# Performance work log

Hardware: AMD Instinct MI355X
Metric: run time of the kernel (lower is better)

## Reference

```python
import jax, jax.numpy as jnp
import numpy as np
jax.config.update('jax_enable_x64', True)

B, T, D = 4, 4096, 1024
H, NX = 16, 16          # num_heads, num_x_bits
NV = D // H             # num_v_bits = 64


def setup_inputs() -> dict:
    key = jax.random.key(0)
    ks = jax.random.split(key, 4)
    s = 1.0 / np.sqrt(D)
    x = jax.random.normal(ks[0], (B, T, D), dtype=jnp.float32)
    Wq = jax.random.uniform(ks[1], (H * NX, D), jnp.float32, -s, s)
    Wk = jax.random.uniform(ks[2], (H * NX, D), jnp.float32, -s, s)
    Wv = jax.random.uniform(ks[3], (H * NV, D), jnp.float32, -s, s)
    emb0 = jnp.full((D,), -1e-5, dtype=jnp.float32)
    emb1 = jnp.full((D,), +1e-5, dtype=jnp.float32)
    return {"x": x, "Wq": Wq, "Wk": Wk, "Wv": Wv, "emb0": emb0, "emb1": emb1}


def _pack_bits(z, nb):
    # z: (B,T,H*nb) -> int64 codes (B,H,T); bit i set iff z_bit_i > 0
    bits = (z > 0).reshape(B, T, H, nb).transpose(0, 2, 1, 3).astype(jnp.int64)
    w = jnp.left_shift(jnp.int64(1), jnp.arange(nb, dtype=jnp.int64))
    return jnp.sum(bits * w, axis=-1)


def _rosa_lookup(qc, kc, vc):
    # Hash-based causal exact-match lookup (inferred semantics of
    # torch_rosa.rosa_qkv_fwd): y[t] = v[j] for the latest j < t with
    # k-code[j] == q-code[t], else 0.  qc,kc,vc: (BH, T) int64.
    BH = qc.shape[0]
    rows = jnp.arange(BH)
    table = jnp.zeros((BH, 1 << NX), dtype=jnp.int64)

    def step(tab, inp):
        qt, kt, vt = inp  # (BH,)
        y = tab[rows, qt]
        tab = tab.at[rows, kt].set(vt)
        return tab, y

    _, ys = jax.lax.scan(step, table, (qc.T, kc.T, vc.T))
    return ys.T  # (BH, T)


def reference(x, Wq, Wk, Wv, emb0, emb1):
    q = x @ Wq.T  # (B,T,H*NX)
    k = x @ Wk.T
    v = x @ Wv.T  # (B,T,H*NV)
    qc = _pack_bits(q, NX).reshape(-1, T)
    kc = _pack_bits(k, NX).reshape(-1, T)
    vc = _pack_bits(v, NV).reshape(-1, T)
    y = _rosa_lookup(qc, kc, vc).reshape(B, H, T)
    rv = jnp.arange(NV, dtype=jnp.int64)
    m = ((y[..., None] >> rv) & 1).astype(bool)      # (B,H,T,NV)
    m = m.transpose(0, 2, 1, 3).reshape(B, T, D)      # (B,T,D)
    return jnp.where(m, emb1, emb0)
```

## Files before the change

### kernel.cpp

```cpp
#include <hip/hip_runtime.h>
#include <stdint.h>

#define B_   4
#define T_   4096
#define D_   1024
#define H_   16
#define M_   16384
#define NTOT 1536
#define BM   64
#define BN   64
#define BK   32
#define KC   384

typedef unsigned short u16;
typedef unsigned long long u64;

__device__ __forceinline__ float bf16r(float f) {
    unsigned int u = __float_as_uint(f);
    u += 0x7FFFu + ((u >> 16) & 1u);
    return __uint_as_float(u & 0xFFFF0000u);
}

__global__ __launch_bounds__(256) void gemm_pack_kernel(
    const float* __restrict__ x, const float* __restrict__ Wq,
    const float* __restrict__ Wk, const float* __restrict__ Wv,
    u16* __restrict__ qc, u16* __restrict__ kc, u64* __restrict__ vc)
{
    __shared__ float As[BM][BK + 1];
    __shared__ float Bs[BK][BN + 4];
    __shared__ unsigned char sub[BM][16];

    const int tid = threadIdx.x;
    const int tx = tid & 15, ty = tid >> 4;
    const int m0 = blockIdx.x * BM;
    const int n0 = blockIdx.y * BN;

    const float* Wsrc; int f0;
    if (n0 < 256)      { Wsrc = Wq; f0 = n0; }
    else if (n0 < 512) { Wsrc = Wk; f0 = n0 - 256; }
    else               { Wsrc = Wv; f0 = n0 - 512; }

    float run[4][4], tot[4][4];
    #pragma unroll
    for (int i = 0; i < 4; ++i)
        #pragma unroll
        for (int j = 0; j < 4; ++j) { run[i][j] = 0.f; tot[i][j] = 0.f; }

    const int r8 = tid >> 2;
    const int c8 = (tid & 3) * 8;

    for (int k0 = 0; k0 < D_; k0 += BK) {
        const float* xp = x + (size_t)(m0 + r8) * D_ + k0 + c8;
        float4 a0 = *(const float4*)xp, a1 = *(const float4*)(xp + 4);
        const float* wp = Wsrc + (size_t)(f0 + r8) * D_ + k0 + c8;
        float4 w0 = *(const float4*)wp, w1 = *(const float4*)(wp + 4);
        As[r8][c8 + 0] = a0.x; As[r8][c8 + 1] = a0.y;
        As[r8][c8 + 2] = a0.z; As[r8][c8 + 3] = a0.w;
        As[r8][c8 + 4] = a1.x; As[r8][c8 + 5] = a1.y;
        As[r8][c8 + 6] = a1.z; As[r8][c8 + 7] = a1.w;
        Bs[c8 + 0][r8] = w0.x; Bs[c8 + 1][r8] = w0.y;
        Bs[c8 + 2][r8] = w0.z; Bs[c8 + 3][r8] = w0.w;
        Bs[c8 + 4][r8] = w1.x; Bs[c8 + 5][r8] = w1.y;
        Bs[c8 + 6][r8] = w1.z; Bs[c8 + 7][r8] = w1.w;
        __syncthreads();

        #pragma unroll 4
        for (int k = 0; k < BK; ++k) {
            float a_[4], b_[4];
            #pragma unroll
            for (int i = 0; i < 4; ++i) a_[i] = As[ty * 4 + i][k];
            #pragma unroll
            for (int j = 0; j < 4; ++j) b_[j] = Bs[k][tx * 4 + j];
            #pragma unroll
            for (int i = 0; i < 4; ++i)
                #pragma unroll
                for (int j = 0; j < 4; ++j)
                    run[i][j] = __builtin_fmaf(a_[i], b_[j], run[i][j]);
        }
        __syncthreads();

        const int kend = k0 + BK;
        if (kend == KC || kend == 2 * KC) {
            #pragma unroll
            for (int i = 0; i < 4; ++i)
                #pragma unroll
                for (int j = 0; j < 4; ++j) {
                    tot[i][j] = tot[i][j] + run[i][j];
                    run[i][j] = 0.f;
                }
        }
    }

    #pragma unroll
    for (int i = 0; i < 4; ++i) {
        unsigned char byte = 0;
        #pragma unroll
        for (int j = 0; j < 4; ++j) {
            float v = tot[i][j] + run[i][j];
            byte |= (unsigned char)((v > 0.0f) ? (1u << j) : 0u);
        }
        sub[ty * 4 + i][tx] = byte;
    }
    __syncthreads();

    if (tid < 64) {
        u64 row = 0ULL;
        #pragma unroll
        for (int c = 0; c < 16; ++c)
            row |= (u64)(sub[tid][c] & 0xFu) << (c * 4);
        const int m = m0 + tid;
        const int b = m >> 12;
        const int t = m & (T_ - 1);
        if (n0 < 512) {
            u16* dst = (n0 < 256) ? qc : kc;
            const int hb = (n0 & 255) >> 4;
            #pragma unroll
            for (int g = 0; g < 4; ++g)
                dst[((size_t)(b * H_ + hb + g)) * T_ + t] = (u16)((row >> (g * 16)) & 0xFFFFULL);
        } else {
            const int h = (n0 - 512) >> 6;
            vc[((size_t)(b * H_ + h)) * T_ + t] = row;
        }
    }
}

__global__ __launch_bounds__(256) void resolve_expand_kernel(
    const u16* __restrict__ qc, const u16* __restrict__ kc,
    const u64* __restrict__ vc,
    const float* __restrict__ emb0, const float* __restrict__ emb1,
    float* __restrict__ out)
{
    __shared__ u16 keys[T_];
    __shared__ u16 pos[T_];
    __shared__ unsigned int cnt[256];
    __shared__ unsigned int offs[257];
    __shared__ float e_lo[64], e_hi[64];

    const int bh = blockIdx.x;
    const int b = bh >> 4, h = bh & 15;
    const u16* kck = kc + (size_t)bh * T_;
    const u16* qck = qc + (size_t)bh * T_;
    const u64* vck = vc + (size_t)bh * T_;
    const int tid = threadIdx.x;

    if (tid < 64) {
        e_lo[tid] = bf16r(emb0[h * 64 + tid]);
        e_hi[tid] = bf16r(emb1[h * 64 + tid]);
    }
    cnt[tid] = 0;
    __syncthreads();
    for (int t = tid; t < T_; t += 256) {
        u16 kv = kck[t];
        keys[t] = kv;
        atomicAdd(&cnt[kv & 255], 1u);
    }
    __syncthreads();
    if (tid == 0) {
        unsigned int s = 0;
        for (int i = 0; i < 256; ++i) { offs[i] = s; s += cnt[i]; }
        offs[256] = s;
    }
    __syncthreads();
    cnt[tid] = offs[tid];
    __syncthreads();
    for (int t = tid; t < T_; t += 256) {
        unsigned int p = atomicAdd(&cnt[keys[t] & 255], 1u);
        pos[p] = (u16)t;
    }
    __syncthreads();
    for (int t = tid; t < T_; t += 256) {
        u16 code = qck[t];
        const int bkt = code & 255;
        int best = -1;
        const unsigned int s = offs[bkt], e = offs[bkt + 1];
        for (unsigned int it = s; it < e; ++it) {
            int j = (int)pos[it];
            if (j < t && keys[j] == code && j > best) best = j;
        }
        u64 yv = (best >= 0) ? vck[best] : 0ULL;
        float* orow = out + ((size_t)(b * T_ + t)) * D_ + h * 64;
        #pragma unroll
        for (int e2 = 0; e2 < 64; ++e2)
            orow[e2] = ((yv >> e2) & 1ULL) ? e_hi[e2] : e_lo[e2];
    }
}

extern "C" void kernel_launch(void* const* d_in, const int* in_sizes, int n_in,
                              void* d_out, int out_size, void* d_ws, size_t ws_size,
                              hipStream_t stream)
{
    const float* x  = (const float*)d_in[0];
    const float* Wq = (const float*)d_in[1];
    const float* Wk = (const float*)d_in[2];
    const float* Wv = (const float*)d_in[3];
    const float* e0 = (const float*)d_in[4];
    const float* e1 = (const float*)d_in[5];

    char* ws = (char*)d_ws;
    u16* qc = (u16*)(ws + 0);
    u16* kc = (u16*)(ws + 524288);
    u64* vc = (u64*)(ws + 1048576);
    float* out = (float*)d_out;

    dim3 gA(M_ / BM, NTOT / BN);
    gemm_pack_kernel<<<gA, 256, 0, stream>>>(x, Wq, Wk, Wv, qc, kc, vc);
    resolve_expand_kernel<<<64, 256, 0, stream>>>(qc, kc, vc, e0, e1, out);
}
```

Before: 811.7 us.

## Enlarge GEMM tiles to 128x128 with 8x8 register blocking and vector LDS reads

```diff
diff --git a/kernel.cpp b/kernel.cpp
--- a/kernel.cpp
+++ b/kernel.cpp
@@ -7,9 +7,9 @@
 #define H_   16
 #define M_   16384
 #define NTOT 1536
-#define BM   64
-#define BN   64
-#define BK   32
+#define BM   128
+#define BN   128
+#define BKK  16
 #define KC   384
 
 typedef unsigned short u16;
@@ -26,65 +26,69 @@
     const float* __restrict__ Wk, const float* __restrict__ Wv,
     u16* __restrict__ qc, u16* __restrict__ kc, u64* __restrict__ vc)
 {
-    __shared__ float As[BM][BK + 1];
-    __shared__ float Bs[BK][BN + 4];
-    __shared__ unsigned char sub[BM][16];
+    __shared__ float As[BKK][BM + 4];
+    __shared__ float Bs[BKK][BN + 4];
+    __shared__ unsigned char sb[BM][33];
 
     const int tid = threadIdx.x;
-    const int tx = tid & 15, ty = tid >> 4;
-    const int m0 = blockIdx.x * BM;
-    const int n0 = blockIdx.y * BN;
+    const int tx = tid & 15;
+    const int ty = tid >> 4;
+    const int n0 = blockIdx.x * BN;
+    const int m0 = blockIdx.y * BM;
 
     const float* Wsrc; int f0;
     if (n0 < 256)      { Wsrc = Wq; f0 = n0; }
     else if (n0 < 512) { Wsrc = Wk; f0 = n0 - 256; }
     else               { Wsrc = Wv; f0 = n0 - 512; }
 
-    float run[4][4], tot[4][4];
+    float run[8][8], tot[8][8];
     #pragma unroll
-    for (int i = 0; i < 4; ++i)
-        #pragma unroll
-        for (int j = 0; j < 4; ++j) { run[i][j] = 0.f; tot[i][j] = 0.f; }
-
-    const int r8 = tid >> 2;
-    const int c8 = (tid & 3) * 8;
-
-    for (int k0 = 0; k0 < D_; k0 += BK) {
-        const float* xp = x + (size_t)(m0 + r8) * D_ + k0 + c8;
-        float4 a0 = *(const float4*)xp, a1 = *(const float4*)(xp + 4);
-        const float* wp = Wsrc + (size_t)(f0 + r8) * D_ + k0 + c8;
-        float4 w0 = *(const float4*)wp, w1 = *(const float4*)(wp + 4);
-        As[r8][c8 + 0] = a0.x; As[r8][c8 + 1] = a0.y;
-        As[r8][c8 + 2] = a0.z; As[r8][c8 + 3] = a0.w;
-        As[r8][c8 + 4] = a1.x; As[r8][c8 + 5] = a1.y;
-        As[r8][c8 + 6] = a1.z; As[r8][c8 + 7] = a1.w;
-        Bs[c8 + 0][r8] = w0.x; Bs[c8 + 1][r8] = w0.y;
-        Bs[c8 + 2][r8] = w0.z; Bs[c8 + 3][r8] = w0.w;
-        Bs[c8 + 4][r8] = w1.x; Bs[c8 + 5][r8] = w1.y;
-        Bs[c8 + 6][r8] = w1.z; Bs[c8 + 7][r8] = w1.w;
+    for (int i = 0; i < 8; ++i)
+        #pragma unroll
+        for (int j = 0; j < 8; ++j) { run[i][j] = 0.f; tot[i][j] = 0.f; }
+
+    for (int k0 = 0; k0 < D_; k0 += BKK) {
+        #pragma unroll
+        for (int l = 0; l < 2; ++l) {
+            const int idx = tid + l * 256;
+            const int r  = idx >> 2;
+            const int c4 = (idx & 3) * 4;
+            float4 xa = *(const float4*)&x[(size_t)(m0 + r) * D_ + k0 + c4];
+            As[c4 + 0][r] = xa.x; As[c4 + 1][r] = xa.y;
+            As[c4 + 2][r] = xa.z; As[c4 + 3][r] = xa.w;
+            float4 wa = *(const float4*)&Wsrc[(size_t)(f0 + r) * D_ + k0 + c4];
+            Bs[c4 + 0][r] = wa.x; Bs[c4 + 1][r] = wa.y;
+            Bs[c4 + 2][r] = wa.z; Bs[c4 + 3][r] = wa.w;
+        }
         __syncthreads();
 
-        #pragma unroll 4
-        for (int k = 0; k < BK; ++k) {
-            float a_[4], b_[4];
-            #pragma unroll
-            for (int i = 0; i < 4; ++i) a_[i] = As[ty * 4 + i][k];
-            #pragma unroll
-            for (int j = 0; j < 4; ++j) b_[j] = Bs[k][tx * 4 + j];
-            #pragma unroll
-            for (int i = 0; i < 4; ++i)
-                #pragma unroll
-                for (int j = 0; j < 4; ++j)
-                    run[i][j] = __builtin_fmaf(a_[i], b_[j], run[i][j]);
+        #pragma unroll
+        for (int k = 0; k < BKK; ++k) {
+            float4 a0 = *(const float4*)&As[k][ty * 4];
+            float4 a1 = *(const float4*)&As[k][64 + ty * 4];
+            float4 b0 = *(const float4*)&Bs[k][tx * 4];
+            float4 b1 = *(const float4*)&Bs[k][64 + tx * 4];
+#define FMAROW(I, AV)                                                     \
+            run[I][0] = __builtin_fmaf(AV, b0.x, run[I][0]);              \
+            run[I][1] = __builtin_fmaf(AV, b0.y, run[I][1]);              \
+            run[I][2] = __builtin_fmaf(AV, b0.z, run[I][2]);              \
+            run[I][3] = __builtin_fmaf(AV, b0.w, run[I][3]);              \
+            run[I][4] = __builtin_fmaf(AV, b1.x, run[I][4]);              \
+            run[I][5] = __builtin_fmaf(AV, b1.y, run[I][5]);              \
+            run[I][6] = __builtin_fmaf(AV, b1.z, run[I][6]);              \
+            run[I][7] = __builtin_fmaf(AV, b1.w, run[I][7]);
+            FMAROW(0, a0.x) FMAROW(1, a0.y) FMAROW(2, a0.z) FMAROW(3, a0.w)
+            FMAROW(4, a1.x) FMAROW(5, a1.y) FMAROW(6, a1.z) FMAROW(7, a1.w)
+#undef FMAROW
         }
         __syncthreads();
 
-        const int kend = k0 + BK;
+        const int kend = k0 + BKK;
         if (kend == KC || kend == 2 * KC) {
             #pragma unroll
-            for (int i = 0; i < 4; ++i)
+            for (int i = 0; i < 8; ++i)
                 #pragma unroll
-                for (int j = 0; j < 4; ++j) {
+                for (int j = 0; j < 8; ++j) {
                     tot[i][j] = tot[i][j] + run[i][j];
                     run[i][j] = 0.f;
                 }
@@ -92,34 +96,44 @@
     }
 
     #pragma unroll
-    for (int i = 0; i < 4; ++i) {
-        unsigned char byte = 0;
+    for (int i = 0; i < 8; ++i) {
+        const int r = (i < 4) ? (ty * 4 + i) : (64 + ty * 4 + (i - 4));
+        unsigned char lo4 = 0, hi4 = 0;
         #pragma unroll
         for (int j = 0; j < 4; ++j) {
-            float v = tot[i][j] + run[i][j];
-            byte |= (unsigned char)((v > 0.0f) ? (1u << j) : 0u);
-        }
-        sub[ty * 4 + i][tx] = byte;
-    }
-    __syncthreads();
-
-    if (tid < 64) {
-        u64 row = 0ULL;
-        #pragma unroll
-        for (int c = 0; c < 16; ++c)
-            row |= (u64)(sub[tid][c] & 0xFu) << (c * 4);
-        const int m = m0 + tid;
+            float vl = tot[i][j] + run[i][j];
+            float vh = tot[i][j + 4] + run[i][j + 4];
+            lo4 |= (unsigned char)((vl > 0.0f) ? (1u << j) : 0u);
+            hi4 |= (unsigned char)((vh > 0.0f) ? (1u << j) : 0u);
+        }
+        sb[r][tx] = lo4;
+        sb[r][16 + tx] = hi4;
+    }
+    __syncthreads();
+
+    if (tid < BM) {
+        const int r = tid;
+        u64 lo = 0ULL, hi = 0ULL;
+        #pragma unroll
+        for (int nb = 0; nb < 16; ++nb) {
+            lo |= (u64)(sb[r][nb] & 0xFu) << (nb * 4);
+            hi |= (u64)(sb[r][16 + nb] & 0xFu) << (nb * 4);
+        }
+        const int m = m0 + r;
         const int b = m >> 12;
         const int t = m & (T_ - 1);
         if (n0 < 512) {
             u16* dst = (n0 < 256) ? qc : kc;
             const int hb = (n0 & 255) >> 4;
             #pragma unroll
-            for (int g = 0; g < 4; ++g)
-                dst[((size_t)(b * H_ + hb + g)) * T_ + t] = (u16)((row >> (g * 16)) & 0xFFFFULL);
+            for (int g = 0; g < 4; ++g) {
+                dst[((size_t)(b * H_ + hb + g)) * T_ + t]     = (u16)((lo >> (g * 16)) & 0xFFFFULL);
+                dst[((size_t)(b * H_ + hb + 4 + g)) * T_ + t] = (u16)((hi >> (g * 16)) & 0xFFFFULL);
+            }
         } else {
-            const int h = (n0 - 512) >> 6;
-            vc[((size_t)(b * H_ + h)) * T_ + t] = row;
+            const int h0 = (n0 - 512) >> 6;
+            vc[((size_t)(b * H_ + h0)) * T_ + t]     = lo;
+            vc[((size_t)(b * H_ + h0 + 1)) * T_ + t] = hi;
         }
     }
 }
@@ -202,7 +216,7 @@
     u64* vc = (u64*)(ws + 1048576);
     float* out = (float*)d_out;
 
-    dim3 gA(M_ / BM, NTOT / BN);
+    dim3 gA(NTOT / BN, M_ / BM);
     gemm_pack_kernel<<<gA, 256, 0, stream>>>(x, Wq, Wk, Wv, qc, kc, vc);
-    resolve_expand_kernel<<<64, 256, 0, stream>>>(qc, kc, vc, e0, e1, out);
-}
+    resolve_expand_kernel<<<B_ * H_, 256, 0, stream>>>(qc, kc, vc, e0, e1, out);
+}
```

Result: slower. 880.3 us (+8.4%).
